# Performance work log

Measured on AMD Instinct MI355X. Metric: run time of the kernel, lower is better.

The kernel has to match this reference:

```python
import jax, jax.numpy as jnp
import numpy as np

EPS = 1e-12
ALPHA = 0.5


def mlp(x, W1, b1, W2, b2):
    # 2-layer MLP (dropout inactive in eval mode) + row-wise l2 norm * 10
    h = jax.nn.relu(x @ W1 + b1)
    y = h @ W2 + b2
    n = jnp.maximum(jnp.linalg.norm(y, axis=-1, keepdims=True), EPS)
    return y / n * 10.0


def setup_inputs() -> dict:
    key = jax.random.key(0)
    ks = jax.random.split(key, 12)
    T, N, F = 3, 100000, 128
    M, E = 4, 65536
    B, H, O = 65536, 128, 64
    X = jax.random.normal(ks[0], (T, N, F), dtype=jnp.float32)
    s_features = jax.random.normal(ks[1], (B, F), dtype=jnp.float32)
    features_map = jax.random.randint(ks[2], (T, N), 0, N)
    s_idxs = jax.random.randint(ks[3], (M, T, E), 0, B)
    t_idxs = jax.random.randint(ks[4], (M, T, E), 0, N)
    weightss = jax.random.uniform(ks[5], (M, T, E), dtype=jnp.float32)
    W1 = jax.random.normal(ks[6], (F, H), dtype=jnp.float32) / np.sqrt(F)
    b1 = jnp.zeros((H,), dtype=jnp.float32)
    W2 = jax.random.normal(ks[7], (H, O), dtype=jnp.float32) / np.sqrt(H)
    b2 = jnp.zeros((O,), dtype=jnp.float32)
    metapath_weights = jnp.ones((M,), dtype=jnp.float32)
    ntype_weights = jnp.ones((T,), dtype=jnp.float32)
    return {"X": X, "s_features": s_features, "features_map": features_map,
            "s_idxs": s_idxs, "t_idxs": t_idxs, "weightss": weightss,
            "batch_size": B, "W1": W1, "b1": b1, "W2": W2, "b2": b2,
            "metapath_weights": metapath_weights, "ntype_weights": ntype_weights}


def reference(X, s_features, features_map, s_idxs, t_idxs, weightss,
              batch_size, W1, b1, W2, b2, metapath_weights, ntype_weights):
    M, T, E = s_idxs.shape
    O = W2.shape[1]
    nm = jax.nn.softmax(metapath_weights)  # [M]
    nt = jax.nn.softmax(ntype_weights)     # [T]
    t_arr = jnp.arange(T)[None, :, None]   # [1,T,1]
    map_idx = features_map[t_arr, t_idxs]  # [M,T,E]
    feats = X[t_arr, map_idx]              # [M,T,E,F] gather
    y = mlp(feats, W1, b1, W2, b2)         # [M,T,E,O]
    # fold metapath & type weights into per-edge weights (scatter is linear)
    ew = weightss * nt[None, :, None] * nm[:, None, None]  # [M,T,E]
    contrib = (y * ew[..., None]).reshape(-1, O)
    seg = s_idxs.reshape(-1)
    out = jax.ops.segment_sum(contrib, seg, num_segments=batch_size)  # [B,O]
    out = (1.0 - ALPHA) * out + ALPHA * mlp(s_features, W1, b1, W2, b2)
    return jax.nn.log_softmax(out, axis=1)
```

## Files before the change

kernel.cpp:

```cpp
#include <hip/hip_runtime.h>

#define Fdim 128
#define Hdim 128
#define Odim 64
#define RT 64
#define ECAP 64
#define EPSV 1e-12f
#define ALPHAV 0.5f

typedef _Float16 h8_t __attribute__((ext_vector_type(8)));
typedef _Float16 h4_t __attribute__((ext_vector_type(4)));
typedef float f32x4 __attribute__((ext_vector_type(4)));

#define W2T_OFF 0
#define X_OFF   16384
#define H_OFF   32768
#define LDS_BYTES 49152
#define WIMG_BYTES 49152

extern "C" __global__ __launch_bounds__(512, 4)
void mlp_all(const float* __restrict__ X, const float* __restrict__ S,
             const char* __restrict__ wimg, const float* __restrict__ b1,
             const float* __restrict__ b2,
             _Float16* __restrict__ Yh, float* __restrict__ out,
             int TN, int rows_total, int ngroups)
{
    extern __shared__ char smem[];
    const int tid  = threadIdx.x;
    const int wave = tid >> 6;
    const int lane = tid & 63;
    const int c = lane & 15;
    const int g = lane >> 4;

    #pragma unroll
    for (int i = 0; i < 2; ++i) {
        int idx = tid + i * 512;
        float4 v = *(const float4*)(wimg + 32768 + idx * 16);
        *(float4*)(smem + W2T_OFF + idx * 16) = v;
    }

    h8_t w1f[4];
    {
        int r0 = wave * 16 + c;
        #pragma unroll
        for (int kt = 0; kt < 4; ++kt)
            w1f[kt] = *(const h8_t*)(wimg + (((r0 << 8) + (kt << 6) + (g << 4)) ^ ((c & 7) << 4)));
    }

    const int hbase = wave * 16 + 4 * g;
    float b1v[4];
    #pragma unroll
    for (int j = 0; j < 4; ++j) b1v[j] = b1[hbase + j];
    float bb[4];
    #pragma unroll
    for (int ct = 0; ct < 4; ++ct) bb[ct] = b2[ct * 16 + c];

    float4 pf[4];
    int grp = blockIdx.x;
    #pragma unroll
    for (int it = 0; it < 4; ++it) {
        int idx = tid + it * 512;
        int r = idx >> 5, c4 = idx & 31;
        int rowg = grp * RT + r;
        float4 v = make_float4(0.f, 0.f, 0.f, 0.f);
        if (rowg < TN)               v = *(const float4*)(X + (size_t)rowg * Fdim + c4 * 4);
        else if (rowg < rows_total)  v = *(const float4*)(S + (size_t)(rowg - TN) * Fdim + c4 * 4);
        pf[it] = v;
    }
    #pragma unroll
    for (int it = 0; it < 4; ++it) {
        int idx = tid + it * 512;
        int r = idx >> 5, c4 = idx & 31;
        h4_t hv;
        hv[0] = (_Float16)pf[it].x; hv[1] = (_Float16)pf[it].y;
        hv[2] = (_Float16)pf[it].z; hv[3] = (_Float16)pf[it].w;
        *(h4_t*)(smem + X_OFF + ((r * 256 + c4 * 8) ^ ((r & 7) << 4))) = hv;
    }
    __syncthreads();

    for (; grp < ngroups; grp += gridDim.x) {
        const int gnext = grp + gridDim.x;

        #pragma unroll
        for (int it = 0; it < 4; ++it) {
            int idx = tid + it * 512;
            int r = idx >> 5, c4 = idx & 31;
            int rowg = gnext * RT + r;
            float4 v = make_float4(0.f, 0.f, 0.f, 0.f);
            if (rowg < TN)               v = *(const float4*)(X + (size_t)rowg * Fdim + c4 * 4);
            else if (rowg < rows_total)  v = *(const float4*)(S + (size_t)(rowg - TN) * Fdim + c4 * 4);
            pf[it] = v;
        }

        f32x4 acc[4];
        #pragma unroll
        for (int r = 0; r < 4; ++r) acc[r] = (f32x4){0.f, 0.f, 0.f, 0.f};

        #pragma unroll
        for (int kt = 0; kt < 4; ++kt) {
            #pragma unroll
            for (int rt = 0; rt < 4; ++rt) {
                int xr = rt * 16 + c;
                h8_t bf = *(const h8_t*)(smem + X_OFF + ((xr * 256 + kt * 64 + g * 16) ^ ((c & 7) << 4)));
                acc[rt] = __builtin_amdgcn_mfma_f32_16x16x32_f16(w1f[kt], bf, acc[rt], 0, 0, 0);
            }
        }

        #pragma unroll
        for (int rt = 0; rt < 4; ++rt) {
            int xr = rt * 16 + c;
            h4_t hv;
            #pragma unroll
            for (int j = 0; j < 4; ++j) {
                float hval = acc[rt][j] + b1v[j];
                hval = fmaxf(hval, 0.f);
                hv[j] = (_Float16)hval;
            }
            *(h4_t*)(smem + H_OFF + ((xr * 256 + hbase * 2) ^ ((xr & 7) << 4))) = hv;
        }
        __syncthreads();

        if (wave < 4) {
            f32x4 acc2[4];
            #pragma unroll
            for (int ct = 0; ct < 4; ++ct) acc2[ct] = (f32x4){0.f, 0.f, 0.f, 0.f};

            #pragma unroll
            for (int kt = 0; kt < 4; ++kt) {
                int xr = wave * 16 + c;
                h8_t a = *(const h8_t*)(smem + H_OFF + ((xr * 256 + kt * 64 + g * 16) ^ ((xr & 7) << 4)));
                #pragma unroll
                for (int ct = 0; ct < 4; ++ct) {
                    int wr = ct * 16 + c;
                    h8_t bf = *(const h8_t*)(smem + W2T_OFF + ((wr * 256 + kt * 64 + g * 16) ^ ((c & 7) << 4)));
                    acc2[ct] = __builtin_amdgcn_mfma_f32_16x16x32_f16(a, bf, acc2[ct], 0, 0, 0);
                }
            }

            float y[4][4];
            float ssq[4] = {0.f, 0.f, 0.f, 0.f};
            #pragma unroll
            for (int ct = 0; ct < 4; ++ct) {
                #pragma unroll
                for (int j = 0; j < 4; ++j) {
                    float v = acc2[ct][j] + bb[ct];
                    y[ct][j] = v;
                    ssq[j] += v * v;
                }
            }
            #pragma unroll
            for (int j = 0; j < 4; ++j) {
                float s = ssq[j];
                s += __shfl_xor(s, 1);
                s += __shfl_xor(s, 2);
                s += __shfl_xor(s, 4);
                s += __shfl_xor(s, 8);
                float n  = fmaxf(sqrtf(s), EPSV);
                float sc = 10.0f / n;
                int rowg = grp * RT + wave * 16 + 4 * g + j;
                if (rowg < TN) {
                    _Float16* dst = Yh + (size_t)rowg * Odim;
                    #pragma unroll
                    for (int ct = 0; ct < 4; ++ct)
                        dst[ct * 16 + c] = (_Float16)(y[ct][j] * sc);
                } else if (rowg < rows_total) {
                    float* dst = out + (size_t)(rowg - TN) * Odim;
                    #pragma unroll
                    for (int ct = 0; ct < 4; ++ct)
                        dst[ct * 16 + c] = ALPHAV * y[ct][j] * sc;
                }
            }
        }

        #pragma unroll
        for (int it = 0; it < 4; ++it) {
            int idx = tid + it * 512;
            int r = idx >> 5, c4 = idx & 31;
            h4_t hv;
            hv[0] = (_Float16)pf[it].x; hv[1] = (_Float16)pf[it].y;
            hv[2] = (_Float16)pf[it].z; hv[3] = (_Float16)pf[it].w;
            *(h4_t*)(smem + X_OFF + ((r * 256 + c4 * 8) ^ ((r & 7) << 4))) = hv;
        }
        __syncthreads();
    }
}

extern "C" __global__ __launch_bounds__(256)
void prep_weights(const float* __restrict__ W1, const float* __restrict__ W2,
                  char* __restrict__ wimg)
{
    int idx = blockIdx.x * 256 + threadIdx.x;
    if (idx < 16384) {
        int h = idx >> 7, f = idx & 127;
        float v = W1[(size_t)f * Hdim + h];
        int byte = (h * 256 + f * 2) ^ ((h & 7) << 4);
        *(_Float16*)(wimg + byte) = (_Float16)v;
    } else if (idx < 24576) {
        int i2 = idx - 16384;
        int o = i2 >> 7, k = i2 & 127;
        float v = W2[(size_t)k * Odim + o];
        int byte = 32768 + ((o * 256 + k * 2) ^ ((o & 7) << 4));
        *(_Float16*)(wimg + byte) = (_Float16)v;
    }
}

extern "C" __global__ void compute_nmt(const float* __restrict__ mw, const float* __restrict__ tw,
                                       float* __restrict__ nmt, int M, int T)
{
    if (threadIdx.x == 0 && blockIdx.x == 0) {
        float mmax = -1e30f, tmax = -1e30f, msum = 0.f, tsum = 0.f;
        for (int i = 0; i < M; ++i) mmax = fmaxf(mmax, mw[i]);
        for (int i = 0; i < M; ++i) msum += expf(mw[i] - mmax);
        for (int i = 0; i < T; ++i) tmax = fmaxf(tmax, tw[i]);
        for (int i = 0; i < T; ++i) tsum += expf(tw[i] - tmax);
        for (int m = 0; m < M; ++m)
            for (int t = 0; t < T; ++t)
                nmt[m * T + t] = (1.0f - ALPHAV) * (expf(mw[m] - mmax) / msum)
                                                * (expf(tw[t] - tmax) / tsum);
    }
}


extern "C" __global__ __launch_bounds__(256)
void zero_ints(int* __restrict__ p, int n)
{
    int i = blockIdx.x * 256 + threadIdx.x;
    if (i < n) p[i] = 0;
}

extern "C" __global__ __launch_bounds__(256)
void scatter_edges(const int* __restrict__ s_idxs, const int* __restrict__ t_idxs,
                   const float* __restrict__ wss, const int* __restrict__ fmap,
                   const float* __restrict__ nmt, int* __restrict__ cnt,
                   int2* __restrict__ edgedat, int Nn, int Tt, int Eslab)
{
    const int slab = blockIdx.y;
    const int t    = slab % Tt;
    const int tN   = t * Nn;
    const float scale = nmt[slab];
    int i = blockIdx.x * 256 + threadIdx.x;
    if (i >= Eslab) return;
    int e = slab * Eslab + i;
    int si   = s_idxs[e];
    int yrow = tN + fmap[tN + t_idxs[e]];
    float w  = wss[e] * scale;
    int pos = atomicAdd(cnt + si, 1);
    if (pos < ECAP)
        edgedat[(size_t)si * ECAP + pos] = make_int2(yrow, __float_as_int(w));
}

extern "C" __global__ __launch_bounds__(256)
void row_gather(const int2* __restrict__ edgedat, const int* __restrict__ cnt,
                const _Float16* __restrict__ Yh, float* __restrict__ out, int B)
{
    const int lane = threadIdx.x & 63;
    const int grp8 = lane >> 3;
    const int sub  = lane & 7;
    int b = blockIdx.x * 4 + (threadIdx.x >> 6);
    if (b >= B) return;
    int n = cnt[b];
    if (n > ECAP) n = ECAP;
    const int2* ebase = edgedat + (size_t)b * ECAP;

    float acc[8];
    #pragma unroll
    for (int j = 0; j < 8; ++j) acc[j] = 0.f;

    for (int e = grp8; e < n; e += 8) {
        int2 ed = ebase[e];
        float w = __int_as_float(ed.y);
        h8_t y8 = *(const h8_t*)(Yh + (size_t)ed.x * Odim + sub * 8);
        #pragma unroll
        for (int j = 0; j < 8; ++j) acc[j] += w * (float)y8[j];
    }
    #pragma unroll
    for (int d = 8; d < 64; d <<= 1) {
        #pragma unroll
        for (int j = 0; j < 8; ++j) acc[j] += __shfl_xor(acc[j], d);
    }
    const float* orow = out + (size_t)b * Odim + sub * 8;
    float v[8];
    #pragma unroll
    for (int j = 0; j < 8; ++j) v[j] = orow[j] + acc[j];

    float mx = v[0];
    #pragma unroll
    for (int j = 1; j < 8; ++j) mx = fmaxf(mx, v[j]);
    #pragma unroll
    for (int d = 1; d < 8; d <<= 1) mx = fmaxf(mx, __shfl_xor(mx, d));
    float sm = 0.f;
    #pragma unroll
    for (int j = 0; j < 8; ++j) sm += expf(v[j] - mx);
    #pragma unroll
    for (int d = 1; d < 8; d <<= 1) sm += __shfl_xor(sm, d);
    float lg = mx + logf(sm);

    if (grp8 == 0) {
        float* dst = out + (size_t)b * Odim + sub * 8;
        #pragma unroll
        for (int j = 0; j < 8; ++j) dst[j] = v[j] - lg;
    }
}


extern "C" __global__ __launch_bounds__(256)
void edge_scatter(const int* __restrict__ s_idxs, const int* __restrict__ t_idxs,
                  const float* __restrict__ weightss, const int* __restrict__ fmap,
                  const _Float16* __restrict__ Yh, const float* __restrict__ nmt,
                  float* __restrict__ out, int Nn, int Tt, int Eslab)
{
    const int lane = threadIdx.x & 63;
    const int slab = blockIdx.y;
    const int t    = slab % Tt;
    const int tN   = t * Nn;
    const float scale = nmt[slab];

    const int wid  = blockIdx.x * (blockDim.x >> 6) + (threadIdx.x >> 6);
    const int off  = wid * 64;
    if (off >= Eslab) return;

    const int ebase = slab * Eslab + off;
    int   e_ok = (off + lane) < Eslab;
    int   eidx = ebase + (e_ok ? lane : 0);
    int   si   = s_idxs[eidx];
    int   ti   = t_idxs[eidx];
    float w    = e_ok ? (weightss[eidx] * scale) : 0.0f;
    int   yrow = tN + fmap[tN + ti];

    #pragma unroll 8
    for (int i = 0; i < 64; ++i) {
        int   nd = __builtin_amdgcn_readlane(yrow, i);
        int   s  = __builtin_amdgcn_readlane(si, i);
        float ws = __uint_as_float(__builtin_amdgcn_readlane(__float_as_uint(w), i));
        float yv = (float)Yh[(size_t)nd * Odim + lane];
        atomicAdd(out + (size_t)s * Odim + lane, yv * ws);
    }
}

extern "C" __global__ __launch_bounds__(256)
void log_softmax_rows(float* __restrict__ out, int Brows)
{
    int lane = threadIdx.x & 63;
    int r = blockIdx.x * 4 + (threadIdx.x >> 6);
    if (r >= Brows) return;
    float* row = out + (size_t)r * Odim;
    float v = row[lane];
    float mx = v;
    for (int off = 32; off > 0; off >>= 1) mx = fmaxf(mx, __shfl_xor(mx, off));
    float ex = expf(v - mx);
    float s = ex;
    for (int off = 32; off > 0; off >>= 1) s += __shfl_xor(s, off);
    row[lane] = v - mx - logf(s);
}

extern "C" void kernel_launch(void* const* d_in, const int* in_sizes, int n_in,
                              void* d_out, int out_size, void* d_ws, size_t ws_size,
                              hipStream_t stream)
{
    const float* X   = (const float*)d_in[0];
    const float* S   = (const float*)d_in[1];
    const int*   fmap= (const int*)d_in[2];
    const int*   sidx= (const int*)d_in[3];
    const int*   tidx= (const int*)d_in[4];
    const float* wss = (const float*)d_in[5];
    const float* W1  = (const float*)d_in[7];
    const float* b1  = (const float*)d_in[8];
    const float* W2  = (const float*)d_in[9];
    const float* b2  = (const float*)d_in[10];
    const float* mw  = (const float*)d_in[11];
    const float* tw  = (const float*)d_in[12];
    float* out = (float*)d_out;

    const int M = in_sizes[11];
    const int T = in_sizes[12];
    const int H = in_sizes[8];
    const int Fv = in_sizes[7] / H;
    const int N = in_sizes[2] / T;
    const int nedges = in_sizes[3];
    const int E = nedges / (M * T);
    const int B = in_sizes[1] / Fv;
    const int TN = T * N;
    const int rows_total = TN + B;
    const int ngroups = (rows_total + RT - 1) / RT;

    char* wp = (char*)d_ws;
    size_t used = 0;
    auto alloc = [&](size_t bytes) -> char* {
        char* p = wp + used;
        used = (used + bytes + 255) & ~(size_t)255;
        return p;
    };
    _Float16* Yh   = (_Float16*)alloc((size_t)TN * Odim * sizeof(_Float16));
    float*    nmt  = (float*)   alloc((size_t)M * T * sizeof(float));
    char*     wimg = (char*)    alloc((size_t)WIMG_BYTES);
    int*      cntp = (int*)     alloc((size_t)B * sizeof(int));
    int2*     edat = (int2*)    alloc((size_t)B * ECAP * sizeof(int2));
    bool bucket_ok = used <= ws_size;

    hipFuncSetAttribute((const void*)mlp_all,
                        hipFuncAttributeMaxDynamicSharedMemorySize, LDS_BYTES);

    compute_nmt<<<1, 64, 0, stream>>>(mw, tw, nmt, M, T);
    prep_weights<<<96, 256, 0, stream>>>(W1, W2, wimg);

    if (bucket_ok) {
        zero_ints<<<(B + 255) / 256, 256, 0, stream>>>(cntp, B);
        dim3 sg((E + 255) / 256, M * T);
        scatter_edges<<<sg, 256, 0, stream>>>(sidx, tidx, wss, fmap, nmt, cntp,
                                              edat, N, T, E);
        mlp_all<<<512, 512, LDS_BYTES, stream>>>(X, S, wimg, b1, b2,
                                                 Yh, out, TN, rows_total, ngroups);
        row_gather<<<(B + 3) / 4, 256, 0, stream>>>(edat, cntp, Yh, out, B);
    } else {
        mlp_all<<<512, 512, LDS_BYTES, stream>>>(X, S, wimg, b1, b2,
                                                 Yh, out, TN, rows_total, ngroups);
        int waves_per_slab = (E + 63) / 64;
        dim3 sg((waves_per_slab + 3) / 4, M * T);
        edge_scatter<<<sg, 256, 0, stream>>>(sidx, tidx, wss, fmap, Yh, nmt, out,
                                             N, T, E);
        log_softmax_rows<<<(B + 3) / 4, 256, 0, stream>>>(out, B);
    }
}
```

Baseline: 149.0 us.

## Fuse edge bucketing into MLP kernel via dedicated blocks and warp-specialize X loads

Merges compute_nmt, zero_ints, and scatter_edges into other kernels. Sixty-four blocks of the MLP launch now do edge bucketing and compute the softmax weights inline. The remaining blocks run the MLP, with the upper four waves doing all X prefetch and fp16 conversion while the lower four do the second GEMM. The aim is to cut launch count and overlap the atomic-heavy bucketing with the memory-bound MLP. The risk is fewer MLP blocks and an uneven split of load work across waves.

```diff
diff --git a/kernel.cpp b/kernel.cpp
--- a/kernel.cpp
+++ b/kernel.cpp
@@ -5,6 +5,7 @@
 #define Odim 64
 #define RT 64
 #define ECAP 64
+#define NSCAT 64
 #define EPSV 1e-12f
 #define ALPHAV 0.5f
 
@@ -19,18 +20,53 @@
 #define WIMG_BYTES 49152
 
 extern "C" __global__ __launch_bounds__(512, 4)
-void mlp_all(const float* __restrict__ X, const float* __restrict__ S,
-             const char* __restrict__ wimg, const float* __restrict__ b1,
-             const float* __restrict__ b2,
-             _Float16* __restrict__ Yh, float* __restrict__ out,
-             int TN, int rows_total, int ngroups)
-{
+void fused_mlp_scatter(const float* __restrict__ X, const float* __restrict__ S,
+                       const char* __restrict__ wimg, const float* __restrict__ b1,
+                       const float* __restrict__ b2,
+                       _Float16* __restrict__ Yh, float* __restrict__ out,
+                       int TN, int rows_total, int ngroups,
+                       const int* __restrict__ s_idxs, const int* __restrict__ t_idxs,
+                       const float* __restrict__ wss, const int* __restrict__ fmap,
+                       const float* __restrict__ mw, const float* __restrict__ tw,
+                       int* __restrict__ cnt, int2* __restrict__ edat,
+                       int Nn, int Tt, int Mm, int Eslab)
+{
+    const int tid = threadIdx.x;
+
+    if (blockIdx.x < NSCAT) {
+        if (edat == nullptr) return;
+        float mmax = -1e30f, tmax = -1e30f, msum = 0.f, tsum = 0.f;
+        for (int i = 0; i < Mm; ++i) mmax = fmaxf(mmax, mw[i]);
+        for (int i = 0; i < Mm; ++i) msum += expf(mw[i] - mmax);
+        for (int i = 0; i < Tt; ++i) tmax = fmaxf(tmax, tw[i]);
+        for (int i = 0; i < Tt; ++i) tsum += expf(tw[i] - tmax);
+        const float inv = (1.0f - ALPHAV) / (msum * tsum);
+
+        const int MT = Mm * Tt;
+        for (int slab = 0; slab < MT; ++slab) {
+            const int t  = slab % Tt;
+            const int tN = t * Nn;
+            const float scale = expf(mw[slab / Tt] - mmax) * expf(tw[t] - tmax) * inv;
+            for (int i = blockIdx.x * 512 + tid; i < Eslab; i += NSCAT * 512) {
+                int e    = slab * Eslab + i;
+                int si   = s_idxs[e];
+                int yrow = tN + fmap[tN + t_idxs[e]];
+                float w  = wss[e] * scale;
+                int pos  = atomicAdd(cnt + si, 1);
+                if (pos < ECAP)
+                    edat[(size_t)si * ECAP + pos] = make_int2(yrow, __float_as_int(w));
+            }
+        }
+        return;
+    }
+
     extern __shared__ char smem[];
-    const int tid  = threadIdx.x;
     const int wave = tid >> 6;
     const int lane = tid & 63;
     const int c = lane & 15;
     const int g = lane >> 4;
+    const bool hi = wave >= 4;
+    const int htid = tid & 255;
 
     #pragma unroll
     for (int i = 0; i < 2; ++i) {
@@ -55,42 +91,48 @@
     #pragma unroll
     for (int ct = 0; ct < 4; ++ct) bb[ct] = b2[ct * 16 + c];
 
-    float4 pf[4];
-    int grp = blockIdx.x;
-    #pragma unroll
-    for (int it = 0; it < 4; ++it) {
-        int idx = tid + it * 512;
-        int r = idx >> 5, c4 = idx & 31;
-        int rowg = grp * RT + r;
-        float4 v = make_float4(0.f, 0.f, 0.f, 0.f);
-        if (rowg < TN)               v = *(const float4*)(X + (size_t)rowg * Fdim + c4 * 4);
-        else if (rowg < rows_total)  v = *(const float4*)(S + (size_t)(rowg - TN) * Fdim + c4 * 4);
-        pf[it] = v;
-    }
-    #pragma unroll
-    for (int it = 0; it < 4; ++it) {
-        int idx = tid + it * 512;
-        int r = idx >> 5, c4 = idx & 31;
-        h4_t hv;
-        hv[0] = (_Float16)pf[it].x; hv[1] = (_Float16)pf[it].y;
-        hv[2] = (_Float16)pf[it].z; hv[3] = (_Float16)pf[it].w;
-        *(h4_t*)(smem + X_OFF + ((r * 256 + c4 * 8) ^ ((r & 7) << 4))) = hv;
-    }
-    __syncthreads();
-
-    for (; grp < ngroups; grp += gridDim.x) {
-        const int gnext = grp + gridDim.x;
-
-        #pragma unroll
-        for (int it = 0; it < 4; ++it) {
-            int idx = tid + it * 512;
+    int grp = blockIdx.x - NSCAT;
+    const int gstride = gridDim.x - NSCAT;
+
+    float4 pf[8];
+    if (hi) {
+        #pragma unroll
+        for (int it = 0; it < 8; ++it) {
+            int idx = htid + it * 256;
             int r = idx >> 5, c4 = idx & 31;
-            int rowg = gnext * RT + r;
+            int rowg = grp * RT + r;
             float4 v = make_float4(0.f, 0.f, 0.f, 0.f);
             if (rowg < TN)               v = *(const float4*)(X + (size_t)rowg * Fdim + c4 * 4);
             else if (rowg < rows_total)  v = *(const float4*)(S + (size_t)(rowg - TN) * Fdim + c4 * 4);
             pf[it] = v;
         }
+        #pragma unroll
+        for (int it = 0; it < 8; ++it) {
+            int idx = htid + it * 256;
+            int r = idx >> 5, c4 = idx & 31;
+            h4_t hv;
+            hv[0] = (_Float16)pf[it].x; hv[1] = (_Float16)pf[it].y;
+            hv[2] = (_Float16)pf[it].z; hv[3] = (_Float16)pf[it].w;
+            *(h4_t*)(smem + X_OFF + ((r * 256 + c4 * 8) ^ ((r & 7) << 4))) = hv;
+        }
+    }
+    __syncthreads();
+
+    for (; grp < ngroups; grp += gstride) {
+        const int gnext = grp + gstride;
+
+        if (hi) {
+            #pragma unroll
+            for (int it = 0; it < 8; ++it) {
+                int idx = htid + it * 256;
+                int r = idx >> 5, c4 = idx & 31;
+                int rowg = gnext * RT + r;
+                float4 v = make_float4(0.f, 0.f, 0.f, 0.f);
+                if (rowg < TN)               v = *(const float4*)(X + (size_t)rowg * Fdim + c4 * 4);
+                else if (rowg < rows_total)  v = *(const float4*)(S + (size_t)(rowg - TN) * Fdim + c4 * 4);
+                pf[it] = v;
+            }
+        }
 
         f32x4 acc[4];
         #pragma unroll
@@ -120,7 +162,7 @@
         }
         __syncthreads();
 
-        if (wave < 4) {
+        if (!hi) {
             f32x4 acc2[4];
             #pragma unroll
             for (int ct = 0; ct < 4; ++ct) acc2[ct] = (f32x4){0.f, 0.f, 0.f, 0.f};
@@ -170,83 +212,43 @@
                         dst[ct * 16 + c] = ALPHAV * y[ct][j] * sc;
                 }
             }
-        }
-
-        #pragma unroll
-        for (int it = 0; it < 4; ++it) {
-            int idx = tid + it * 512;
-            int r = idx >> 5, c4 = idx & 31;
-            h4_t hv;
-            hv[0] = (_Float16)pf[it].x; hv[1] = (_Float16)pf[it].y;
-            hv[2] = (_Float16)pf[it].z; hv[3] = (_Float16)pf[it].w;
-            *(h4_t*)(smem + X_OFF + ((r * 256 + c4 * 8) ^ ((r & 7) << 4))) = hv;
+        } else {
+            #pragma unroll
+            for (int it = 0; it < 8; ++it) {
+                int idx = htid + it * 256;
+                int r = idx >> 5, c4 = idx & 31;
+                h4_t hv;
+                hv[0] = (_Float16)pf[it].x; hv[1] = (_Float16)pf[it].y;
+                hv[2] = (_Float16)pf[it].z; hv[3] = (_Float16)pf[it].w;
+                *(h4_t*)(smem + X_OFF + ((r * 256 + c4 * 8) ^ ((r & 7) << 4))) = hv;
+            }
         }
         __syncthreads();
     }
 }
 
 extern "C" __global__ __launch_bounds__(256)
-void prep_weights(const float* __restrict__ W1, const float* __restrict__ W2,
-                  char* __restrict__ wimg)
-{
-    int idx = blockIdx.x * 256 + threadIdx.x;
-    if (idx < 16384) {
-        int h = idx >> 7, f = idx & 127;
-        float v = W1[(size_t)f * Hdim + h];
-        int byte = (h * 256 + f * 2) ^ ((h & 7) << 4);
-        *(_Float16*)(wimg + byte) = (_Float16)v;
-    } else if (idx < 24576) {
-        int i2 = idx - 16384;
-        int o = i2 >> 7, k = i2 & 127;
-        float v = W2[(size_t)k * Odim + o];
-        int byte = 32768 + ((o * 256 + k * 2) ^ ((o & 7) << 4));
-        *(_Float16*)(wimg + byte) = (_Float16)v;
-    }
-}
-
-extern "C" __global__ void compute_nmt(const float* __restrict__ mw, const float* __restrict__ tw,
-                                       float* __restrict__ nmt, int M, int T)
-{
-    if (threadIdx.x == 0 && blockIdx.x == 0) {
-        float mmax = -1e30f, tmax = -1e30f, msum = 0.f, tsum = 0.f;
-        for (int i = 0; i < M; ++i) mmax = fmaxf(mmax, mw[i]);
-        for (int i = 0; i < M; ++i) msum += expf(mw[i] - mmax);
-        for (int i = 0; i < T; ++i) tmax = fmaxf(tmax, tw[i]);
-        for (int i = 0; i < T; ++i) tsum += expf(tw[i] - tmax);
-        for (int m = 0; m < M; ++m)
-            for (int t = 0; t < T; ++t)
-                nmt[m * T + t] = (1.0f - ALPHAV) * (expf(mw[m] - mmax) / msum)
-                                                * (expf(tw[t] - tmax) / tsum);
-    }
-}
-
-
-extern "C" __global__ __launch_bounds__(256)
-void zero_ints(int* __restrict__ p, int n)
-{
-    int i = blockIdx.x * 256 + threadIdx.x;
-    if (i < n) p[i] = 0;
-}
-
-extern "C" __global__ __launch_bounds__(256)
-void scatter_edges(const int* __restrict__ s_idxs, const int* __restrict__ t_idxs,
-                   const float* __restrict__ wss, const int* __restrict__ fmap,
-                   const float* __restrict__ nmt, int* __restrict__ cnt,
-                   int2* __restrict__ edgedat, int Nn, int Tt, int Eslab)
-{
-    const int slab = blockIdx.y;
-    const int t    = slab % Tt;
-    const int tN   = t * Nn;
-    const float scale = nmt[slab];
-    int i = blockIdx.x * 256 + threadIdx.x;
-    if (i >= Eslab) return;
-    int e = slab * Eslab + i;
-    int si   = s_idxs[e];
-    int yrow = tN + fmap[tN + t_idxs[e]];
-    float w  = wss[e] * scale;
-    int pos = atomicAdd(cnt + si, 1);
-    if (pos < ECAP)
-        edgedat[(size_t)si * ECAP + pos] = make_int2(yrow, __float_as_int(w));
+void prep_all(const float* __restrict__ W1, const float* __restrict__ W2,
+              char* __restrict__ wimg, int* __restrict__ cnt, int B)
+{
+    if (blockIdx.x < 96) {
+        int idx = blockIdx.x * 256 + threadIdx.x;
+        if (idx < 16384) {
+            int h = idx >> 7, f = idx & 127;
+            float v = W1[(size_t)f * Hdim + h];
+            int byte = (h * 256 + f * 2) ^ ((h & 7) << 4);
+            *(_Float16*)(wimg + byte) = (_Float16)v;
+        } else if (idx < 24576) {
+            int i2 = idx - 16384;
+            int o = i2 >> 7, k = i2 & 127;
+            float v = W2[(size_t)k * Odim + o];
+            int byte = 32768 + ((o * 256 + k * 2) ^ ((o & 7) << 4));
+            *(_Float16*)(wimg + byte) = (_Float16)v;
+        }
+    } else {
+        int i = (blockIdx.x - 96) * 256 + threadIdx.x;
+        if (i < B) cnt[i] = 0;
+    }
 }
 
 extern "C" __global__ __launch_bounds__(256)
@@ -306,14 +308,21 @@
 extern "C" __global__ __launch_bounds__(256)
 void edge_scatter(const int* __restrict__ s_idxs, const int* __restrict__ t_idxs,
                   const float* __restrict__ weightss, const int* __restrict__ fmap,
-                  const _Float16* __restrict__ Yh, const float* __restrict__ nmt,
-                  float* __restrict__ out, int Nn, int Tt, int Eslab)
+                  const _Float16* __restrict__ Yh, const float* __restrict__ mw,
+                  const float* __restrict__ tw,
+                  float* __restrict__ out, int Nn, int Tt, int Mm, int Eslab)
 {
     const int lane = threadIdx.x & 63;
     const int slab = blockIdx.y;
     const int t    = slab % Tt;
     const int tN   = t * Nn;
-    const float scale = nmt[slab];
+    float mmax = -1e30f, tmax = -1e30f, msum = 0.f, tsum = 0.f;
+    for (int i = 0; i < Mm; ++i) mmax = fmaxf(mmax, mw[i]);
+    for (int i = 0; i < Mm; ++i) msum += expf(mw[i] - mmax);
+    for (int i = 0; i < Tt; ++i) tmax = fmaxf(tmax, tw[i]);
+    for (int i = 0; i < Tt; ++i) tsum += expf(tw[i] - tmax);
+    const float scale = (1.0f - ALPHAV) * expf(mw[slab / Tt] - mmax) * expf(tw[t] - tmax)
+                        / (msum * tsum);
 
     const int wid  = blockIdx.x * (blockDim.x >> 6) + (threadIdx.x >> 6);
     const int off  = wid * 64;
@@ -391,33 +400,30 @@
         return p;
     };
     _Float16* Yh   = (_Float16*)alloc((size_t)TN * Odim * sizeof(_Float16));
-    float*    nmt  = (float*)   alloc((size_t)M * T * sizeof(float));
     char*     wimg = (char*)    alloc((size_t)WIMG_BYTES);
     int*      cntp = (int*)     alloc((size_t)B * sizeof(int));
     int2*     edat = (int2*)    alloc((size_t)B * ECAP * sizeof(int2));
     bool bucket_ok = used <= ws_size;
 
-    hipFuncSetAttribute((const void*)mlp_all,
+    hipFuncSetAttribute((const void*)fused_mlp_scatter,
                         hipFuncAttributeMaxDynamicSharedMemorySize, LDS_BYTES);
 
-    compute_nmt<<<1, 64, 0, stream>>>(mw, tw, nmt, M, T);
-    prep_weights<<<96, 256, 0, stream>>>(W1, W2, wimg);
+    const int zb = (B + 255) / 256;
+    prep_all<<<96 + zb, 256, 0, stream>>>(W1, W2, wimg, cntp, B);
 
     if (bucket_ok) {
-        zero_ints<<<(B + 255) / 256, 256, 0, stream>>>(cntp, B);
-        dim3 sg((E + 255) / 256, M * T);
-        scatter_edges<<<sg, 256, 0, stream>>>(sidx, tidx, wss, fmap, nmt, cntp,
-                                              edat, N, T, E);
-        mlp_all<<<512, 512, LDS_BYTES, stream>>>(X, S, wimg, b1, b2,
-                                                 Yh, out, TN, rows_total, ngroups);
+        fused_mlp_scatter<<<NSCAT + 448, 512, LDS_BYTES, stream>>>(
+            X, S, wimg, b1, b2, Yh, out, TN, rows_total, ngroups,
+            sidx, tidx, wss, fmap, mw, tw, cntp, edat, N, T, M, E);
         row_gather<<<(B + 3) / 4, 256, 0, stream>>>(edat, cntp, Yh, out, B);
     } else {
-        mlp_all<<<512, 512, LDS_BYTES, stream>>>(X, S, wimg, b1, b2,
-                                                 Yh, out, TN, rows_total, ngroups);
+        fused_mlp_scatter<<<NSCAT + 448, 512, LDS_BYTES, stream>>>(
+            X, S, wimg, b1, b2, Yh, out, TN, rows_total, ngroups,
+            sidx, tidx, wss, fmap, mw, tw, cntp, nullptr, N, T, M, E);
         int waves_per_slab = (E + 63) / 64;
         dim3 sg((waves_per_slab + 3) / 4, M * T);
-        edge_scatter<<<sg, 256, 0, stream>>>(sidx, tidx, wss, fmap, Yh, nmt, out,
-                                             N, T, E);
+        edge_scatter<<<sg, 256, 0, stream>>>(sidx, tidx, wss, fmap, Yh, mw, tw, out,
+                                             N, T, M, E);
         log_softmax_rows<<<(B + 3) / 4, 256, 0, stream>>>(out, B);
     }
 }
```

After: 175.7 us. +17.9%, slower.
